# Optimization experiments

Hardware: AMD Instinct MI355X
Metric: run time of the kernel (lower is better)

## Reference

```python
import jax, jax.numpy as jnp
import numpy as np

NUM_EMBEDDINGS = 8192
EMBEDDING_DIM = 512
COMMITMENT_COST = 0.25
N_INPUTS = 32768


def setup_inputs() -> dict:
    key = jax.random.key(0)
    k1, k2 = jax.random.split(key)
    inputs = jax.random.normal(k1, (N_INPUTS, EMBEDDING_DIM), dtype=jnp.float32)
    weight = jax.random.normal(k2, (NUM_EMBEDDINGS, EMBEDDING_DIM), dtype=jnp.float32)
    return {"inputs": inputs, "weight": weight}


def reference(inputs, weight):
    # distances[n, k] = ||x_n||^2 + ||w_k||^2 - 2 x_n . w_k   -> [N, K]
    distances = (
        jnp.sum(inputs ** 2, axis=1, keepdims=True)
        + jnp.sum(weight ** 2, axis=1)
        - 2.0 * (inputs @ weight.T)
    )
    probs = jax.nn.softmax(-distances, axis=-1)            # [N, K]
    idx = jnp.argmin(distances, axis=1)                    # [N]
    quantized = weight[idx]                                # gather == one-hot @ weight

    e_latent_loss = jnp.mean((jax.lax.stop_gradient(quantized) - inputs) ** 2)
    q_latent_loss = jnp.mean((quantized - jax.lax.stop_gradient(inputs)) ** 2)
    loss = q_latent_loss + COMMITMENT_COST * e_latent_loss

    # straight-through estimator
    quantized_st = inputs + jax.lax.stop_gradient(quantized - inputs)

    # avg over one-hot encodings == normalized code histogram
    counts = jnp.bincount(idx, length=NUM_EMBEDDINGS).astype(inputs.dtype)
    avg_probs = counts / inputs.shape[0]
    perplexity = jnp.exp(-jnp.sum(avg_probs * jnp.log(avg_probs + 1e-10)))

    return (quantized_st, probs, loss, perplexity)
```

## Files before the change

### kernel.cpp

```cpp
#include <hip/hip_runtime.h>
#include <hip/hip_fp16.h>
#include <math.h>

#define N_ROWS 32768
#define K_CODES 8192
#define DIM 512

#define OUT_Q 0
#define OUT_P ((size_t)N_ROWS * DIM)
#define OUT_LOSS (OUT_P + (size_t)N_ROWS * K_CODES)
#define OUT_PERP (OUT_LOSS + 1)

#define WS_WSQ 0
#define WS_CNT (K_CODES)
#define WS_ERR (2 * K_CODES)
#define WS_F16 (2 * K_CODES + N_ROWS)

#define XH_OFF ((size_t)0)
#define XL_OFF ((size_t)N_ROWS * DIM)
#define WH_OFF ((size_t)2 * N_ROWS * DIM)
#define WL_OFF ((size_t)2 * N_ROWS * DIM + (size_t)K_CODES * DIM)
#define F16_COUNT ((size_t)2 * (N_ROWS + K_CODES) * DIM)
#define WS_NEEDED ((size_t)WS_F16 * 4 + F16_COUNT * 2)

typedef _Float16 f16x8 __attribute__((ext_vector_type(8)));
typedef float f32x4 __attribute__((ext_vector_type(4)));

__device__ inline void load_lds16(const void* g, void* l) {
    __builtin_amdgcn_global_load_lds((const __attribute__((address_space(1))) void*)g,
                                     (__attribute__((address_space(3))) void*)l,
                                     16, 0, 0);
}

__device__ inline unsigned int fkey(float f) {
    unsigned int b = __float_as_uint(f);
    return b ^ ((unsigned int)((int)b >> 31) | 0x80000000u);
}
__device__ inline float fkey_inv(unsigned int k) {
    unsigned int b = (k & 0x80000000u) ? (k ^ 0x80000000u) : ~k;
    return __uint_as_float(b);
}

__global__ void wsq_kernel(const float* __restrict__ W, float* __restrict__ ws) {
    int row = blockIdx.x;
    int lane = threadIdx.x;
    const float* src = W + (size_t)row * DIM;
    float4 v0 = *(const float4*)(src + lane * 8);
    float4 v1 = *(const float4*)(src + lane * 8 + 4);
    float s = v0.x * v0.x + v0.y * v0.y + v0.z * v0.z + v0.w * v0.w
            + v1.x * v1.x + v1.y * v1.y + v1.z * v1.z + v1.w * v1.w;
#pragma unroll
    for (int off = 32; off > 0; off >>= 1) s += __shfl_down(s, off, 64);
    if (lane == 0) ws[WS_WSQ + row] = s;
}

__global__ void __launch_bounds__(256) convert_split_kernel(
    const float* __restrict__ X, const float* __restrict__ W,
    _Float16* __restrict__ f16base, float* __restrict__ ws) {
    const size_t NX8 = (size_t)N_ROWS * DIM / 8;
    size_t t = (size_t)blockIdx.x * 256 + threadIdx.x;
    const float* src;
    _Float16 *hd, *ld;
    bool isW = (t >= NX8);
    if (!isW) {
        src = X + t * 8;
        hd = f16base + XH_OFF + t * 8;
        ld = f16base + XL_OFF + t * 8;
    } else {
        size_t u = t - NX8;
        src = W + u * 8;
        hd = f16base + WH_OFF + u * 8;
        ld = f16base + WL_OFF + u * 8;
    }
    float4 v0 = *(const float4*)src;
    float4 v1 = *(const float4*)(src + 4);
    float v[8] = {v0.x, v0.y, v0.z, v0.w, v1.x, v1.y, v1.z, v1.w};
    f16x8 h, l;
    float s = 0.f;
#pragma unroll
    for (int i = 0; i < 8; ++i) {
        _Float16 hv = (_Float16)v[i];
        h[i] = hv;
        l[i] = (_Float16)(v[i] - (float)hv);
        s += v[i] * v[i];
    }
    *(f16x8*)hd = h;
    *(f16x8*)ld = l;
    if (isW) {
#pragma unroll
        for (int off = 32; off > 0; off >>= 1) s += __shfl_down(s, off, 64);
        if ((threadIdx.x & 63) == 0) ws[WS_WSQ + ((t - NX8) >> 6)] = s;
    }
}

#define LDSB 24576
#define AH_O 0
#define AL_O 8192
#define BH_O 16384
#define BL_O 20480

__global__ void __launch_bounds__(512, 2) gemm_dist_mfma_kernel(
    const _Float16* __restrict__ f16base, const float* __restrict__ ws,
    float* __restrict__ out) {
    __shared__ _Float16 lds[3 * LDSB];

    const int tid = threadIdx.x;
    const int w = tid >> 6;
    const int lane = tid & 63;

    int lin = blockIdx.y * 64 + blockIdx.x;
    int swz = (lin & 7) * 1024 + (lin >> 3);
    const int bn = (swz & 63) * 128;
    const int bm = (swz >> 6) * 256;

    const int wr = w >> 1;
    const int wc = w & 1;
    const int q = lane >> 4;
    const int fm = lane & 15;
    const int l4 = lane >> 2;
    const int p = lane & 3;

    f32x4 acc[4][4];
#pragma unroll
    for (int i = 0; i < 4; ++i)
#pragma unroll
        for (int j = 0; j < 4; ++j) acc[i][j] = (f32x4){0.f, 0.f, 0.f, 0.f};

    auto stage = [&](int ks, _Float16* buf, int part) {
        const int kk = ks * 32;
        int g = w * 2 + part;
        int arow = g * 16 + l4;
        int ca = p ^ ((arow >> 1) & 3);
        size_t aoff = (size_t)(bm + arow) * DIM + kk + ca * 8;
        load_lds16(f16base + XH_OFF + aoff, buf + AH_O + g * 512);
        load_lds16(f16base + XL_OFF + aoff, buf + AL_O + g * 512);
        int brow = w * 16 + l4;
        int cb = p ^ ((brow >> 1) & 3);
        size_t boff = (size_t)(bn + brow) * DIM + kk + cb * 8;
        if (part == 0)
            load_lds16(f16base + WH_OFF + boff, buf + BH_O + w * 512);
        else
            load_lds16(f16base + WL_OFF + boff, buf + BL_O + w * 512);
    };

    _Float16* c0 = lds;
    _Float16* c1 = lds + LDSB;
    _Float16* c2 = lds + 2 * LDSB;

    stage(0, c0, 0); stage(0, c0, 1);
    stage(1, c1, 0); stage(1, c1, 1);
    asm volatile("s_waitcnt vmcnt(6)" ::: "memory");
    __builtin_amdgcn_s_barrier();
    __builtin_amdgcn_sched_barrier(0);

#pragma unroll 1
    for (int ks = 0; ks < 16; ++ks) {
        f16x8 bhv[4], blv[4];
#pragma unroll
        for (int j = 0; j < 4; ++j) {
            int bb = wc * 64 + j * 16 + fm;
            int off = bb * 32 + ((q ^ ((bb >> 1) & 3)) * 8);
            bhv[j] = *(const f16x8*)&c0[BH_O + off];
            blv[j] = *(const f16x8*)&c0[BL_O + off];
        }
        f16x8 ah[2], al[2];
#pragma unroll
        for (int i = 0; i < 2; ++i) {
            int am = wr * 64 + i * 16 + fm;
            int off = am * 32 + ((q ^ ((am >> 1) & 3)) * 8);
            ah[i] = *(const f16x8*)&c0[AH_O + off];
            al[i] = *(const f16x8*)&c0[AL_O + off];
        }
        if (ks < 14) stage(ks + 2, c2, 0);
        __builtin_amdgcn_s_setprio(1);
#pragma unroll
        for (int i = 0; i < 2; ++i)
#pragma unroll
            for (int j = 0; j < 4; ++j) {
                acc[i][j] = __builtin_amdgcn_mfma_f32_16x16x32_f16(
                    ah[i], bhv[j], acc[i][j], 0, 0, 0);
                acc[i][j] = __builtin_amdgcn_mfma_f32_16x16x32_f16(
                    ah[i], blv[j], acc[i][j], 0, 0, 0);
                acc[i][j] = __builtin_amdgcn_mfma_f32_16x16x32_f16(
                    al[i], bhv[j], acc[i][j], 0, 0, 0);
            }
        __builtin_amdgcn_s_setprio(0);
        __builtin_amdgcn_s_barrier();
        __builtin_amdgcn_sched_barrier(0);

#pragma unroll
        for (int i = 0; i < 2; ++i) {
            int am = wr * 64 + (i + 2) * 16 + fm;
            int off = am * 32 + ((q ^ ((am >> 1) & 3)) * 8);
            ah[i] = *(const f16x8*)&c0[AH_O + off];
            al[i] = *(const f16x8*)&c0[AL_O + off];
        }
        if (ks < 14) stage(ks + 2, c2, 1);
        __builtin_amdgcn_s_setprio(1);
#pragma unroll
        for (int i = 0; i < 2; ++i)
#pragma unroll
            for (int j = 0; j < 4; ++j) {
                acc[i + 2][j] = __builtin_amdgcn_mfma_f32_16x16x32_f16(
                    ah[i], bhv[j], acc[i + 2][j], 0, 0, 0);
                acc[i + 2][j] = __builtin_amdgcn_mfma_f32_16x16x32_f16(
                    ah[i], blv[j], acc[i + 2][j], 0, 0, 0);
                acc[i + 2][j] = __builtin_amdgcn_mfma_f32_16x16x32_f16(
                    al[i], bhv[j], acc[i + 2][j], 0, 0, 0);
            }
        __builtin_amdgcn_s_setprio(0);
        if (ks < 14) {
            asm volatile("s_waitcnt vmcnt(6)" ::: "memory");
        } else if (ks == 14) {
            asm volatile("s_waitcnt vmcnt(0)" ::: "memory");
        }
        __builtin_amdgcn_s_barrier();
        __builtin_amdgcn_sched_barrier(0);

        _Float16* t0 = c0; c0 = c1; c1 = c2; c2 = t0;
    }

    const float* wsq = ws + WS_WSQ;
    float* Dout = out + OUT_P;
    const int q4 = q * 4;
#pragma unroll
    for (int i = 0; i < 4; ++i) {
#pragma unroll
        for (int j = 0; j < 4; ++j) {
            int n = bn + wc * 64 + j * 16 + fm;
            float wn = wsq[n];
#pragma unroll
            for (int r = 0; r < 4; ++r) {
                int m = bm + wr * 64 + i * 16 + q4 + r;
                Dout[(size_t)m * K_CODES + n] = wn - 2.f * acc[i][j][r];
            }
        }
    }
}

#define BM 128
#define BN 128
#define BK 16

__global__ void __launch_bounds__(256) gemm_dist_fp32_kernel(
    const float* __restrict__ X, const float* __restrict__ W,
    const float* __restrict__ ws, float* __restrict__ out) {
    __shared__ float As[BK][BM];
    __shared__ float Bs[BK][BN];

    const int bn = blockIdx.x * BN;
    const int bm = blockIdx.y * BM;
    const int tid = threadIdx.x;
    const int tx = tid & 15;
    const int ty = tid >> 4;
    const int lr = tid >> 1;
    const int lc = (tid & 1) * 8;

    float acc[8][8];
#pragma unroll
    for (int i = 0; i < 8; ++i)
#pragma unroll
        for (int j = 0; j < 8; ++j) acc[i][j] = 0.f;

    const float* aptr = X + (size_t)(bm + lr) * DIM + lc;
    const float* bptr = W + (size_t)(bn + lr) * DIM + lc;

    for (int k0 = 0; k0 < DIM; k0 += BK) {
        float4 a0 = *(const float4*)(aptr + k0);
        float4 a1 = *(const float4*)(aptr + k0 + 4);
        float4 b0 = *(const float4*)(bptr + k0);
        float4 b1 = *(const float4*)(bptr + k0 + 4);
        __syncthreads();
        As[lc + 0][lr] = a0.x; As[lc + 1][lr] = a0.y;
        As[lc + 2][lr] = a0.z; As[lc + 3][lr] = a0.w;
        As[lc + 4][lr] = a1.x; As[lc + 5][lr] = a1.y;
        As[lc + 6][lr] = a1.z; As[lc + 7][lr] = a1.w;
        Bs[lc + 0][lr] = b0.x; Bs[lc + 1][lr] = b0.y;
        Bs[lc + 2][lr] = b0.z; Bs[lc + 3][lr] = b0.w;
        Bs[lc + 4][lr] = b1.x; Bs[lc + 5][lr] = b1.y;
        Bs[lc + 6][lr] = b1.z; Bs[lc + 7][lr] = b1.w;
        __syncthreads();
#pragma unroll
        for (int kk = 0; kk < BK; ++kk) {
            float a[8], b[8];
            *(float4*)&a[0] = *(const float4*)&As[kk][ty * 8];
            *(float4*)&a[4] = *(const float4*)&As[kk][ty * 8 + 4];
            *(float4*)&b[0] = *(const float4*)&Bs[kk][tx * 8];
            *(float4*)&b[4] = *(const float4*)&Bs[kk][tx * 8 + 4];
#pragma unroll
            for (int i = 0; i < 8; ++i)
#pragma unroll
                for (int j = 0; j < 8; ++j)
                    acc[i][j] = fmaf(a[i], b[j], acc[i][j]);
        }
    }

    const float* wsq = ws + WS_WSQ;
    const int m0 = bm + ty * 8;
    const int n0 = bn + tx * 8;
    float wn[8];
    *(float4*)&wn[0] = *(const float4*)(wsq + n0);
    *(float4*)&wn[4] = *(const float4*)(wsq + n0 + 4);
    float* Dout = out + OUT_P;
#pragma unroll
    for (int i = 0; i < 8; ++i) {
        float4 o0, o1;
        o0.x = wn[0] - 2.f * acc[i][0];
        o0.y = wn[1] - 2.f * acc[i][1];
        o0.z = wn[2] - 2.f * acc[i][2];
        o0.w = wn[3] - 2.f * acc[i][3];
        o1.x = wn[4] - 2.f * acc[i][4];
        o1.y = wn[5] - 2.f * acc[i][5];
        o1.z = wn[6] - 2.f * acc[i][6];
        o1.w = wn[7] - 2.f * acc[i][7];
        float* drow = Dout + (size_t)(m0 + i) * K_CODES + n0;
        *(float4*)(drow) = o0;
        *(float4*)(drow + 4) = o1;
    }
}

__global__ void __launch_bounds__(256) probs_quant_kernel(
    const float* __restrict__ X, const float* __restrict__ W,
    float* __restrict__ out, float* __restrict__ ws) {
    const int n = blockIdx.x;
    const int tid = threadIdx.x;
    __shared__ unsigned long long mred[4];
    __shared__ float fred[4];

    float4* Drow4 = (float4*)(out + OUT_P + (size_t)n * K_CODES);

    float4 e[8];
    unsigned long long best = ~0ull;
#pragma unroll
    for (int t = 0; t < 8; ++t) {
        float4 v = Drow4[tid + t * 256];
        e[t] = v;
        unsigned int c0 = (unsigned int)((tid + t * 256) * 4);
        unsigned long long k;
        k = ((unsigned long long)fkey(v.x) << 32) | (c0 + 0u);
        best = k < best ? k : best;
        k = ((unsigned long long)fkey(v.y) << 32) | (c0 + 1u);
        best = k < best ? k : best;
        k = ((unsigned long long)fkey(v.z) << 32) | (c0 + 2u);
        best = k < best ? k : best;
        k = ((unsigned long long)fkey(v.w) << 32) | (c0 + 3u);
        best = k < best ? k : best;
    }
#pragma unroll
    for (int d = 1; d < 64; d <<= 1) {
        unsigned long long o = __shfl_xor(best, d, 64);
        best = o < best ? o : best;
    }
    if ((tid & 63) == 0) mred[tid >> 6] = best;
    __syncthreads();
    unsigned long long bm = mred[0];
    bm = mred[1] < bm ? mred[1] : bm;
    bm = mred[2] < bm ? mred[2] : bm;
    bm = mred[3] < bm ? mred[3] : bm;
    const float smin = fkey_inv((unsigned int)(bm >> 32));
    const int amin = (int)(bm & 0xFFFFFFFFu);

    float sum = 0.f;
#pragma unroll
    for (int t = 0; t < 8; ++t) {
        float4 v = e[t];
        float4 ev;
        ev.x = __expf(smin - v.x);
        ev.y = __expf(smin - v.y);
        ev.z = __expf(smin - v.z);
        ev.w = __expf(smin - v.w);
        e[t] = ev;
        sum += ev.x + ev.y + ev.z + ev.w;
    }
#pragma unroll
    for (int off = 32; off > 0; off >>= 1) sum += __shfl_down(sum, off, 64);
    if ((tid & 63) == 0) fred[tid >> 6] = sum;
    __syncthreads();
    const float inv = 1.0f / (fred[0] + fred[1] + fred[2] + fred[3]);

#pragma unroll
    for (int t = 0; t < 8; ++t) {
        float4 ev = e[t];
        ev.x *= inv; ev.y *= inv; ev.z *= inv; ev.w *= inv;
        Drow4[tid + t * 256] = ev;
    }

    const float2* xr = (const float2*)(X + (size_t)n * DIM);
    const float2* wr = (const float2*)(W + (size_t)amin * DIM);
    float2* qr = (float2*)(out + OUT_Q + (size_t)n * DIM);
    float2 x = xr[tid];
    float2 qv = wr[tid];
    float2 d2, o;
    d2.x = qv.x - x.x; d2.y = qv.y - x.y;
    o.x = x.x + d2.x;  o.y = x.y + d2.y;
    qr[tid] = o;
    float err = d2.x * d2.x + d2.y * d2.y;
#pragma unroll
    for (int off = 32; off > 0; off >>= 1) err += __shfl_down(err, off, 64);
    __syncthreads();
    if ((tid & 63) == 0) fred[tid >> 6] = err;
    __syncthreads();
    if (tid == 0) {
        ws[WS_ERR + n] = fred[0] + fred[1] + fred[2] + fred[3];
        atomicAdd(ws + WS_CNT + amin, 1.0f);
    }
}

__global__ void __launch_bounds__(1024) finalize_kernel(
    float* __restrict__ out, const float* __restrict__ ws) {
    __shared__ float red[1024];
    const int tid = threadIdx.x;

    float errsum = 0.f;
    for (int j = tid; j < N_ROWS; j += 1024) errsum += ws[WS_ERR + j];
    red[tid] = errsum;
    __syncthreads();
    for (int st = 512; st > 0; st >>= 1) {
        if (tid < st) red[tid] += red[tid + st];
        __syncthreads();
    }
    const float total_err = red[0];
    __syncthreads();

    float ent = 0.f;
    for (int j = tid; j < K_CODES; j += 1024) {
        float p = ws[WS_CNT + j] * (1.0f / (float)N_ROWS);
        ent -= p * logf(p + 1e-10f);
    }
    red[tid] = ent;
    __syncthreads();
    for (int st = 512; st > 0; st >>= 1) {
        if (tid < st) red[tid] += red[tid + st];
        __syncthreads();
    }
    if (tid == 0) {
        float mse = total_err * (1.0f / ((float)N_ROWS * (float)DIM));
        out[OUT_LOSS] = mse + 0.25f * mse;
        out[OUT_PERP] = expf(red[0]);
    }
}

extern "C" void kernel_launch(void* const* d_in, const int* in_sizes, int n_in,
                              void* d_out, int out_size, void* d_ws, size_t ws_size,
                              hipStream_t stream) {
    const float* X = (const float*)d_in[0];
    const float* W = (const float*)d_in[1];
    float* out = (float*)d_out;
    float* ws = (float*)d_ws;

    hipMemsetAsync(ws + WS_CNT, 0, K_CODES * sizeof(float), stream);

    if (ws_size >= WS_NEEDED) {
        _Float16* f16base = (_Float16*)(ws + WS_F16);
        const int conv_blocks =
            (int)(((size_t)(N_ROWS + K_CODES) * DIM / 8 + 255) / 256);
        convert_split_kernel<<<conv_blocks, 256, 0, stream>>>(X, W, f16base, ws);

        dim3 ggrid(64, 128);
        gemm_dist_mfma_kernel<<<ggrid, 512, 0, stream>>>(f16base, ws, out);
    } else {
        wsq_kernel<<<K_CODES, 64, 0, stream>>>(W, ws);
        dim3 ggrid(K_CODES / BN, N_ROWS / BM);
        gemm_dist_fp32_kernel<<<ggrid, 256, 0, stream>>>(X, W, ws, out);
    }

    probs_quant_kernel<<<N_ROWS, 256, 0, stream>>>(X, W, out, ws);
    finalize_kernel<<<1, 1024, 0, stream>>>(out, ws);
}
```

Baseline: 2.311 ms.

## Restructure GEMM k-loop, remap block swizzle, widen probs kernel, split finalize

The GEMM main loop now issues both prefetch stages up front and runs all 4x4 MFMA tiles in one phase, dropping the mid-iteration barrier. The block-to-tile swizzle changes so each XCD covers 8 adjacent N tiles. The probs kernel moves to 512 threads per row with fewer registers per thread. The single-block finalize is split into a 32-block partial reduction plus a tiny final kernel. Together these aim to cut barrier stalls, improve L2 locality and shorten the serial tail, at the cost of higher register pressure from holding all A fragments at once and one extra kernel launch.

```diff
diff --git a/kernel.cpp b/kernel.cpp
--- a/kernel.cpp
+++ b/kernel.cpp
@@ -14,7 +14,8 @@
 #define WS_WSQ 0
 #define WS_CNT (K_CODES)
 #define WS_ERR (2 * K_CODES)
-#define WS_F16 (2 * K_CODES + N_ROWS)
+#define WS_RED (2 * K_CODES + N_ROWS)
+#define WS_F16 (2 * K_CODES + N_ROWS + 64)
 
 #define XH_OFF ((size_t)0)
 #define XL_OFF ((size_t)N_ROWS * DIM)
@@ -109,9 +110,10 @@
     const int lane = tid & 63;
 
     int lin = blockIdx.y * 64 + blockIdx.x;
-    int swz = (lin & 7) * 1024 + (lin >> 3);
-    const int bn = (swz & 63) * 128;
-    const int bm = (swz >> 6) * 256;
+    int xcd = lin & 7;
+    int idx = lin >> 3;
+    const int bn = (xcd * 8 + (idx & 7)) * 128;
+    const int bm = (idx >> 3) * 256;
 
     const int wr = w >> 1;
     const int wc = w & 1;
@@ -155,7 +157,9 @@
 
 #pragma unroll 1
     for (int ks = 0; ks < 16; ++ks) {
-        f16x8 bhv[4], blv[4];
+        if (ks < 14) { stage(ks + 2, c2, 0); stage(ks + 2, c2, 1); }
+
+        f16x8 bhv[4], blv[4], ahv[4], alv[4];
 #pragma unroll
         for (int j = 0; j < 4; ++j) {
             int bb = wc * 64 + j * 16 + fm;
@@ -163,52 +167,28 @@
             bhv[j] = *(const f16x8*)&c0[BH_O + off];
             blv[j] = *(const f16x8*)&c0[BL_O + off];
         }
-        f16x8 ah[2], al[2];
-#pragma unroll
-        for (int i = 0; i < 2; ++i) {
+#pragma unroll
+        for (int i = 0; i < 4; ++i) {
             int am = wr * 64 + i * 16 + fm;
             int off = am * 32 + ((q ^ ((am >> 1) & 3)) * 8);
-            ah[i] = *(const f16x8*)&c0[AH_O + off];
-            al[i] = *(const f16x8*)&c0[AL_O + off];
+            ahv[i] = *(const f16x8*)&c0[AH_O + off];
+            alv[i] = *(const f16x8*)&c0[AL_O + off];
         }
-        if (ks < 14) stage(ks + 2, c2, 0);
+
         __builtin_amdgcn_s_setprio(1);
 #pragma unroll
-        for (int i = 0; i < 2; ++i)
+        for (int i = 0; i < 4; ++i)
 #pragma unroll
             for (int j = 0; j < 4; ++j) {
                 acc[i][j] = __builtin_amdgcn_mfma_f32_16x16x32_f16(
-                    ah[i], bhv[j], acc[i][j], 0, 0, 0);
+                    ahv[i], bhv[j], acc[i][j], 0, 0, 0);
                 acc[i][j] = __builtin_amdgcn_mfma_f32_16x16x32_f16(
-                    ah[i], blv[j], acc[i][j], 0, 0, 0);
+                    ahv[i], blv[j], acc[i][j], 0, 0, 0);
                 acc[i][j] = __builtin_amdgcn_mfma_f32_16x16x32_f16(
-                    al[i], bhv[j], acc[i][j], 0, 0, 0);
+                    alv[i], bhv[j], acc[i][j], 0, 0, 0);
             }
         __builtin_amdgcn_s_setprio(0);
-        __builtin_amdgcn_s_barrier();
-        __builtin_amdgcn_sched_barrier(0);
-
-#pragma unroll
-        for (int i = 0; i < 2; ++i) {
-            int am = wr * 64 + (i + 2) * 16 + fm;
-            int off = am * 32 + ((q ^ ((am >> 1) & 3)) * 8);
-            ah[i] = *(const f16x8*)&c0[AH_O + off];
-            al[i] = *(const f16x8*)&c0[AL_O + off];
-        }
-        if (ks < 14) stage(ks + 2, c2, 1);
-        __builtin_amdgcn_s_setprio(1);
-#pragma unroll
-        for (int i = 0; i < 2; ++i)
-#pragma unroll
-            for (int j = 0; j < 4; ++j) {
-                acc[i + 2][j] = __builtin_amdgcn_mfma_f32_16x16x32_f16(
-                    ah[i], bhv[j], acc[i + 2][j], 0, 0, 0);
-                acc[i + 2][j] = __builtin_amdgcn_mfma_f32_16x16x32_f16(
-                    ah[i], blv[j], acc[i + 2][j], 0, 0, 0);
-                acc[i + 2][j] = __builtin_amdgcn_mfma_f32_16x16x32_f16(
-                    al[i], bhv[j], acc[i + 2][j], 0, 0, 0);
-            }
-        __builtin_amdgcn_s_setprio(0);
+
         if (ks < 14) {
             asm volatile("s_waitcnt vmcnt(6)" ::: "memory");
         } else if (ks == 14) {
@@ -319,23 +299,25 @@
     }
 }
 
-__global__ void __launch_bounds__(256) probs_quant_kernel(
+__global__ void __launch_bounds__(512) probs_quant_kernel(
     const float* __restrict__ X, const float* __restrict__ W,
     float* __restrict__ out, float* __restrict__ ws) {
     const int n = blockIdx.x;
     const int tid = threadIdx.x;
-    __shared__ unsigned long long mred[4];
-    __shared__ float fred[4];
+    __shared__ unsigned long long mred[8];
+    __shared__ float fred[8];
 
     float4* Drow4 = (float4*)(out + OUT_P + (size_t)n * K_CODES);
 
-    float4 e[8];
+    const float x = X[(size_t)n * DIM + tid];
+
+    float4 e[4];
     unsigned long long best = ~0ull;
 #pragma unroll
-    for (int t = 0; t < 8; ++t) {
-        float4 v = Drow4[tid + t * 256];
+    for (int t = 0; t < 4; ++t) {
+        float4 v = Drow4[tid + t * 512];
         e[t] = v;
-        unsigned int c0 = (unsigned int)((tid + t * 256) * 4);
+        unsigned int c0 = (unsigned int)((tid + t * 512) * 4);
         unsigned long long k;
         k = ((unsigned long long)fkey(v.x) << 32) | (c0 + 0u);
         best = k < best ? k : best;
@@ -354,15 +336,14 @@
     if ((tid & 63) == 0) mred[tid >> 6] = best;
     __syncthreads();
     unsigned long long bm = mred[0];
-    bm = mred[1] < bm ? mred[1] : bm;
-    bm = mred[2] < bm ? mred[2] : bm;
-    bm = mred[3] < bm ? mred[3] : bm;
+#pragma unroll
+    for (int i = 1; i < 8; ++i) bm = mred[i] < bm ? mred[i] : bm;
     const float smin = fkey_inv((unsigned int)(bm >> 32));
     const int amin = (int)(bm & 0xFFFFFFFFu);
 
     float sum = 0.f;
 #pragma unroll
-    for (int t = 0; t < 8; ++t) {
+    for (int t = 0; t < 4; ++t) {
         float4 v = e[t];
         float4 ev;
         ev.x = __expf(smin - v.x);
@@ -376,67 +357,81 @@
     for (int off = 32; off > 0; off >>= 1) sum += __shfl_down(sum, off, 64);
     if ((tid & 63) == 0) fred[tid >> 6] = sum;
     __syncthreads();
-    const float inv = 1.0f / (fred[0] + fred[1] + fred[2] + fred[3]);
-
-#pragma unroll
-    for (int t = 0; t < 8; ++t) {
+    float tot = fred[0];
+#pragma unroll
+    for (int i = 1; i < 8; ++i) tot += fred[i];
+    const float inv = 1.0f / tot;
+
+#pragma unroll
+    for (int t = 0; t < 4; ++t) {
         float4 ev = e[t];
         ev.x *= inv; ev.y *= inv; ev.z *= inv; ev.w *= inv;
-        Drow4[tid + t * 256] = ev;
-    }
-
-    const float2* xr = (const float2*)(X + (size_t)n * DIM);
-    const float2* wr = (const float2*)(W + (size_t)amin * DIM);
-    float2* qr = (float2*)(out + OUT_Q + (size_t)n * DIM);
-    float2 x = xr[tid];
-    float2 qv = wr[tid];
-    float2 d2, o;
-    d2.x = qv.x - x.x; d2.y = qv.y - x.y;
-    o.x = x.x + d2.x;  o.y = x.y + d2.y;
-    qr[tid] = o;
-    float err = d2.x * d2.x + d2.y * d2.y;
+        Drow4[tid + t * 512] = ev;
+    }
+
+    const float qv = W[(size_t)amin * DIM + tid];
+    out[OUT_Q + (size_t)n * DIM + tid] = qv;
+    float d2 = qv - x;
+    float err = d2 * d2;
 #pragma unroll
     for (int off = 32; off > 0; off >>= 1) err += __shfl_down(err, off, 64);
     __syncthreads();
     if ((tid & 63) == 0) fred[tid >> 6] = err;
     __syncthreads();
     if (tid == 0) {
-        ws[WS_ERR + n] = fred[0] + fred[1] + fred[2] + fred[3];
+        float e8 = fred[0];
+#pragma unroll
+        for (int i = 1; i < 8; ++i) e8 += fred[i];
+        ws[WS_ERR + n] = e8;
         atomicAdd(ws + WS_CNT + amin, 1.0f);
     }
 }
 
-__global__ void __launch_bounds__(1024) finalize_kernel(
-    float* __restrict__ out, const float* __restrict__ ws) {
-    __shared__ float red[1024];
+__global__ void __launch_bounds__(256) finalize_part_kernel(
+    float* __restrict__ ws) {
+    __shared__ float red[256];
+    const int b = blockIdx.x;
     const int tid = threadIdx.x;
 
     float errsum = 0.f;
-    for (int j = tid; j < N_ROWS; j += 1024) errsum += ws[WS_ERR + j];
+    const int ebase = b * 1024;
+#pragma unroll
+    for (int j = tid; j < 1024; j += 256) errsum += ws[WS_ERR + ebase + j];
+
+    float p = ws[WS_CNT + b * 256 + tid] * (1.0f / (float)N_ROWS);
+    float ent = -p * logf(p + 1e-10f);
+
     red[tid] = errsum;
     __syncthreads();
-    for (int st = 512; st > 0; st >>= 1) {
+    for (int st = 128; st > 0; st >>= 1) {
         if (tid < st) red[tid] += red[tid + st];
         __syncthreads();
     }
-    const float total_err = red[0];
-    __syncthreads();
-
-    float ent = 0.f;
-    for (int j = tid; j < K_CODES; j += 1024) {
-        float p = ws[WS_CNT + j] * (1.0f / (float)N_ROWS);
-        ent -= p * logf(p + 1e-10f);
-    }
+    if (tid == 0) ws[WS_RED + b] = red[0];
+    __syncthreads();
     red[tid] = ent;
     __syncthreads();
-    for (int st = 512; st > 0; st >>= 1) {
+    for (int st = 128; st > 0; st >>= 1) {
         if (tid < st) red[tid] += red[tid + st];
         __syncthreads();
     }
+    if (tid == 0) ws[WS_RED + 32 + b] = red[0];
+}
+
+__global__ void __launch_bounds__(64) finalize_fin_kernel(
+    float* __restrict__ out, const float* __restrict__ ws) {
+    const int tid = threadIdx.x;
+    float ev = tid < 32 ? ws[WS_RED + tid] : 0.f;
+    float nv = tid < 32 ? ws[WS_RED + 32 + tid] : 0.f;
+#pragma unroll
+    for (int off = 32; off > 0; off >>= 1) {
+        ev += __shfl_down(ev, off, 64);
+        nv += __shfl_down(nv, off, 64);
+    }
     if (tid == 0) {
-        float mse = total_err * (1.0f / ((float)N_ROWS * (float)DIM));
+        float mse = ev * (1.0f / ((float)N_ROWS * (float)DIM));
         out[OUT_LOSS] = mse + 0.25f * mse;
-        out[OUT_PERP] = expf(red[0]);
+        out[OUT_PERP] = expf(nv);
     }
 }
 
@@ -464,6 +459,7 @@
         gemm_dist_fp32_kernel<<<ggrid, 256, 0, stream>>>(X, W, ws, out);
     }
 
-    probs_quant_kernel<<<N_ROWS, 256, 0, stream>>>(X, W, out, ws);
-    finalize_kernel<<<1, 1024, 0, stream>>>(out, ws);
-}
+    probs_quant_kernel<<<N_ROWS, 512, 0, stream>>>(X, W, out, ws);
+    finalize_part_kernel<<<32, 256, 0, stream>>>(ws);
+    finalize_fin_kernel<<<1, 64, 0, stream>>>(out, ws);
+}
```

Result: no change. 2.349 ms (+1.6%).
